# Kernel optimization log

Hardware: AMD Instinct MI355X
Metric: run time of the kernel (lower is better)

## Reference

```python
import jax, jax.numpy as jnp
import numpy as np

ALPHA = 1.0
NEG = -1e20  # boundary value used by the torch module


def _compute_mu(W, alpha):
    """DTW location parameter mu: [B, Na+1, Nb+1].
    mu[i,j] = alpha*W[i-1,j-1] + logsumexp(mu[i-1,j], mu[i,j-1], mu[i-1,j-1]).
    Row-wise scan (outer over i) with an inner scan over j for the
    left-dependency; fully vectorized over batch.
    """
    B, Na, Nb = W.shape
    aW = alpha * W  # [B, Na, Nb]
    # row 0: mu[:,0,0]=0, mu[:,0,1:]=-1e20
    row0 = jnp.concatenate([jnp.zeros((B, 1), W.dtype),
                            jnp.full((B, Nb), NEG, W.dtype)], axis=1)

    def row_step(prev_row, w_row):  # prev_row [B, Nb+1], w_row [B, Nb]
        up = prev_row[:, 1:]    # mu[i-1, j]   for j=1..Nb -> [B, Nb]
        diag = prev_row[:, :-1]  # mu[i-1, j-1]            -> [B, Nb]

        def col_step(left, inp):
            u, d, w = inp  # each [B]
            val = w + jax.nn.logsumexp(jnp.stack([u, left, d], axis=0), axis=0)
            return val, val

        left0 = jnp.full((B,), NEG, W.dtype)  # mu[i, 0] = -1e20
        xs = (up.T, diag.T, w_row.T)          # scan over Nb
        _, vals = jax.lax.scan(col_step, left0, xs)  # [Nb, B]
        new_row = jnp.concatenate([jnp.full((B, 1), NEG, W.dtype), vals.T], axis=1)
        return new_row, new_row

    _, rows = jax.lax.scan(row_step, row0, jnp.swapaxes(aW, 0, 1))  # [Na, B, Nb+1]
    mu = jnp.concatenate([row0[:, None, :], jnp.swapaxes(rows, 0, 1)], axis=1)
    return mu  # [B, Na+1, Nb+1]


def _compute_pi(W, mu, mask, alpha):
    """Reduced transition tensor pi: [B, Na, Nb, 3] (softmax over moves)."""
    up = mu[:, :-1, 1:]    # mu[i-1, j]
    left = mu[:, 1:, :-1]  # mu[i, j-1]
    diag = mu[:, :-1, :-1]  # mu[i-1, j-1]
    raw = jnp.stack([up, left, diag], axis=-1) + alpha * W[..., None]
    return jax.nn.softmax(raw, axis=-1) * mask


def setup_inputs() -> dict:
    key = jax.random.key(0)
    k1, _ = jax.random.split(key)
    B, Na, Nb = 64, 384, 384
    W = jax.random.normal(k1, (B, Na, Nb), dtype=jnp.float32)
    mask = jnp.ones((B, Na, Nb, 1), dtype=jnp.float32)
    return {"W": W, "mask": mask}


def reference(W, mask):
    mu = _compute_mu(W, ALPHA)
    pi = _compute_pi(W, mu, mask, ALPHA)
    return (mu, pi)
```

## Files before the change

kernel.cpp:

```cpp
#include <hip/hip_runtime.h>

#define NA 384
#define NB 384
#define NBATCH 64
#define NEGV -1e20f
#define C 8
#define NCW 6
#define TOT_CH 56
#define WPITCH 68
#define LOG2E 1.44269504088896340736f
#define LN2   0.69314718055994530942f

typedef float f4 __attribute__((ext_vector_type(4)));

struct alignas(16) SharedT {
    float stage[2][NCW][64 * 9];
    float wtile[2][NCW][8 * WPITCH];
    float bound[NCW - 1][NB + 1];
    int   progress[NCW - 1];
    int   computed[NCW];
    int   drained[NCW][2];
    int   wready[NCW];
};

__device__ __forceinline__ void loadW8(const float* __restrict__ Wb, int rbase,
                                       int kk, int l, float (&r)[8])
{
    const int rl = l >> 3, cc = l & 7;
    const int colb = 8 * kk + cc;
#pragma unroll
    for (int i = 0; i < 8; ++i) {
        const int row = 8 * i + rl;
        int col = colb - row;
        col = col < 0 ? 0 : (col > NB - 1 ? NB - 1 : col);
        r[i] = Wb[(size_t)(rbase + row) * NB + col];
    }
}

template<bool FULL>
__device__ __forceinline__ void chunk_body(int k, int w, int l,
                                           float& val, float& diag, SharedT& sh)
{
    const int s0 = 1 + k * C;

    {
        volatile int* wr = &sh.wready[w];
        while (*wr < k + 1) { }
        __builtin_amdgcn_sched_barrier(0);
        asm volatile("" ::: "memory");
    }
    const float* wt = &sh.wtile[k & 1][w][0];
    const int wb = (l >> 3) * WPITCH + (l & 7) * 8;
    const f4 wlo = *(const f4*)(wt + wb);
    const f4 whi = *(const f4*)(wt + wb + 4);

    if (k >= 2) {
        volatile int* dr = &sh.drained[w][k & 1];
        while (*dr < k - 2) __builtin_amdgcn_s_sleep(1);
        __builtin_amdgcn_sched_barrier(0);
        asm volatile("" ::: "memory");
    }
    if (w > 0 && s0 <= NB) {
        const int need = (s0 + C - 1 < NB) ? s0 + C - 1 : NB;
        volatile int* pr = &sh.progress[w - 1];
        while (*pr < need) { }
        __builtin_amdgcn_sched_barrier(0);
        asm volatile("" ::: "memory");
    }
    float bnd[C];
    if (w > 0) {
#pragma unroll
        for (int c = 0; c < C; ++c) {
            const int s = s0 + c;
            bnd[c] = sh.bound[w - 1][s <= NB ? s : NB];
        }
    }
    float wc[C];
    wc[0] = wlo.x * LOG2E; wc[1] = wlo.y * LOG2E;
    wc[2] = wlo.z * LOG2E; wc[3] = wlo.w * LOG2E;
    wc[4] = whi.x * LOG2E; wc[5] = whi.y * LOG2E;
    wc[6] = whi.z * LOG2E; wc[7] = whi.w * LOG2E;

    float* st = &sh.stage[k & 1][w][0];
    __builtin_amdgcn_s_setprio(1);
#pragma unroll
    for (int c = 0; c < C; ++c) {
        const int s = s0 + c;
        float upv = __int_as_float(__builtin_amdgcn_update_dpp(
            0, __float_as_int(val), 0x138 , 0xF, 0xF, false));
        if (l == 0) upv = (w > 0 && s <= NB) ? bnd[c] : NEGV;
        const int j = s - l;
        if (FULL || (j >= 1 && j <= NB)) {
            const float m  = fmaxf(fmaxf(upv, val), diag);
            const float eu = exp2f(upv  - m);
            const float el = exp2f(val  - m);
            const float ed = exp2f(diag - m);
            const float nv = wc[c] + m + __log2f(eu + el + ed);
            st[l * 9 + c] = nv;
            if (w < NCW - 1 && l == 63) sh.bound[w][j] = nv;
            diag = upv;
            val  = nv;
        }
    }
    asm volatile("s_waitcnt lgkmcnt(0)" ::: "memory");
    if (l == 63) {
        if (w < NCW - 1) {
            const int done = s0 + C - 1 - 63;
            if (done >= 1) *(volatile int*)&sh.progress[w] = done;
        }
        *(volatile int*)&sh.computed[w] = k + 1;
    }
    __builtin_amdgcn_s_setprio(0);
}

template<bool FULL>
__device__ __forceinline__ void io_iter(int k, int cw, int l,
        const float* __restrict__ Wb, int rbase, float* __restrict__ mub,
        SharedT& sh)
{
    float wreg[8];
    const bool prep = (k + 2 < TOT_CH);
    if (prep) loadW8(Wb, rbase, k + 2, l, wreg);

    volatile int* cp = &sh.computed[cw];
    while (*cp < k + 1) __builtin_amdgcn_s_sleep(1);
    __builtin_amdgcn_sched_barrier(0);
    asm volatile("" ::: "memory");

    const float* st = &sh.stage[k & 1][cw][0];
    float v[8];
    const int lr = l >> 3, cc = l & 7;
#pragma unroll
    for (int q = 0; q < 8; ++q) v[q] = st[(lr + 8 * q) * 9 + cc];
    asm volatile("s_waitcnt lgkmcnt(0)" ::: "memory");
    if (l == 0) *(volatile int*)&sh.drained[cw][k & 1] = k;

    if (prep) {
        float* wt = &sh.wtile[k & 1][cw][0];
#pragma unroll
        for (int i = 0; i < 8; ++i) wt[i * WPITCH + l] = wreg[i];
        asm volatile("s_waitcnt lgkmcnt(0)" ::: "memory");
        if (l == 0) *(volatile int*)&sh.wready[cw] = k + 3;
    }

    const int colbase = k * C;
#pragma unroll
    for (int q = 0; q < 8; ++q) {
        const int lrow = lr + 8 * q;
        const int col  = colbase + cc - lrow;
        if (FULL || (col >= 0 && col < NB))
            mub[(size_t)(rbase + lrow + 1) * (NB + 1) + col + 1] = v[q] * LN2;
    }
}

__global__ __launch_bounds__(768, 1) void dtw_mu(const float* __restrict__ W,
                                                 float* __restrict__ mu)
{
    __shared__ SharedT sh;
    const int b = blockIdx.x, tid = threadIdx.x;
    const int w = tid >> 6, l = tid & 63;
    const float* Wb = W + (size_t)b * NA * NB;
    float* mub = mu + (size_t)b * (NA + 1) * (NB + 1);

    if (tid < 384) {
        mub[tid + 1] = NEGV;
        mub[(size_t)(tid + 1) * (NB + 1)] = NEGV;
    }
    if (tid == 0) mub[0] = 0.0f;
    if (tid < NCW - 1) sh.progress[tid] = 0;
    if (tid < NCW) { sh.computed[tid] = 0; sh.wready[tid] = 0; }
    if (tid < 2 * NCW) sh.drained[tid >> 1][tid & 1] = -1;
    __syncthreads();

    if (w < NCW) {
        const int rbase = w << 6;
        float val  = NEGV;
        float diag = (rbase + l == 0) ? 0.0f : NEGV;
        for (int k = 0; k < 8; ++k)       chunk_body<false>(k, w, l, val, diag, sh);
        for (int k = 8; k < 48; ++k)      chunk_body<true >(k, w, l, val, diag, sh);
        for (int k = 48; k < TOT_CH; ++k) chunk_body<false>(k, w, l, val, diag, sh);
    } else {
        const int cw = w - NCW, rbase = cw << 6;
        float wreg[8];
        loadW8(Wb, rbase, 0, l, wreg);
        {
            float* wt = &sh.wtile[0][cw][0];
#pragma unroll
            for (int i = 0; i < 8; ++i) wt[i * WPITCH + l] = wreg[i];
        }
        loadW8(Wb, rbase, 1, l, wreg);
        {
            float* wt = &sh.wtile[1][cw][0];
#pragma unroll
            for (int i = 0; i < 8; ++i) wt[i * WPITCH + l] = wreg[i];
        }
        asm volatile("s_waitcnt lgkmcnt(0)" ::: "memory");
        if (l == 0) *(volatile int*)&sh.wready[cw] = 2;

        for (int k = 0; k < 8; ++k)       io_iter<false>(k, cw, l, Wb, rbase, mub, sh);
        for (int k = 8; k < 48; ++k)      io_iter<true >(k, cw, l, Wb, rbase, mub, sh);
        for (int k = 48; k < TOT_CH; ++k) io_iter<false>(k, cw, l, Wb, rbase, mub, sh);
    }
}

__global__ __launch_bounds__(256) void dtw_pi(const float* __restrict__ W,
        const float* __restrict__ mask, const float* __restrict__ mu,
        float* __restrict__ pi)
{
    const long long idx = ((long long)blockIdx.x * 256 + threadIdx.x) * 4;
    const int rr = (int)(idx / NB);
    const int jj = (int)(idx - (long long)rr * NB);
    const int b  = rr / NA;
    const int ii = rr - b * NA;
    const float* m0 = mu + (size_t)b * (NA + 1) * (NB + 1)
                         + (size_t)ii * (NB + 1) + jj;
    const float* m1 = m0 + (NB + 1);
    const float d0 = m0[0], d1 = m0[1], d2 = m0[2], d3 = m0[3], d4 = m0[4];
    const float L0 = m1[0], L1 = m1[1], L2 = m1[2], L3 = m1[3], L4 = m1[4];
    const f4 wv = *(const f4*)(W + idx);
    const f4 mk = *(const f4*)(mask + idx);

    const float t0 = wv.x - L1, t1 = wv.y - L2, t2 = wv.z - L3, t3 = wv.w - L4;
    f4 o0, o1, o2;
    o0.x = exp2f((d1 + t0) * LOG2E) * mk.x;
    o0.y = exp2f((L0 + t0) * LOG2E) * mk.x;
    o0.z = exp2f((d0 + t0) * LOG2E) * mk.x;
    o0.w = exp2f((d2 + t1) * LOG2E) * mk.y;
    o1.x = exp2f((L1 + t1) * LOG2E) * mk.y;
    o1.y = exp2f((d1 + t1) * LOG2E) * mk.y;
    o1.z = exp2f((d3 + t2) * LOG2E) * mk.z;
    o1.w = exp2f((L2 + t2) * LOG2E) * mk.z;
    o2.x = exp2f((d2 + t2) * LOG2E) * mk.z;
    o2.y = exp2f((d4 + t3) * LOG2E) * mk.w;
    o2.z = exp2f((L3 + t3) * LOG2E) * mk.w;
    o2.w = exp2f((d3 + t3) * LOG2E) * mk.w;

    f4* po = (f4*)(pi + idx * 3);
    po[0] = o0; po[1] = o1; po[2] = o2;
}

extern "C" void kernel_launch(void* const* d_in, const int* in_sizes, int n_in,
                              void* d_out, int out_size, void* d_ws, size_t ws_size,
                              hipStream_t stream) {
    const float* W    = (const float*)d_in[0];
    const float* mask = (const float*)d_in[1];
    float* mu = (float*)d_out;
    float* pi = mu + (size_t)NBATCH * (NA + 1) * (NB + 1);

    hipLaunchKernelGGL(dtw_mu, dim3(NBATCH), dim3(768), 0, stream, W, mu);

    const int cells  = NBATCH * NA * NB;
    const int blocks = cells / (256 * 4);
    hipLaunchKernelGGL(dtw_pi, dim3(blocks), dim3(256), 0, stream,
                       W, mask, mu, pi);
}
```

Baseline: 164.3 us.

## Deepen W prefetch pipeline to four buffers and prefetch next chunk weights early

The shared W tile ring grows from two to four slots. The IO wavefronts keep two chunks of W in registers and issue global loads five chunks ahead, so load latency is hidden behind more work. The compute wavefronts now wait on wready and read the next chunk's weights at the end of the current chunk, which takes that LDS read off the critical path at the start of each chunk. The cost is more LDS and registers, plus an extra spin-wait at the tail of each chunk.

```diff
diff --git a/kernel.cpp b/kernel.cpp
--- a/kernel.cpp
+++ b/kernel.cpp
@@ -15,7 +15,7 @@
 
 struct alignas(16) SharedT {
     float stage[2][NCW][64 * 9];
-    float wtile[2][NCW][8 * WPITCH];
+    float wtile[4][NCW][8 * WPITCH];
     float bound[NCW - 1][NB + 1];
     int   progress[NCW - 1];
     int   computed[NCW];
@@ -37,22 +37,28 @@
     }
 }
 
+__device__ __forceinline__ void writeWt(float* __restrict__ wt,
+                                        const float (&r)[8], int l) {
+#pragma unroll
+    for (int i = 0; i < 8; ++i) wt[i * WPITCH + l] = r[i];
+}
+
+__device__ __forceinline__ void readWc(const float* __restrict__ wt, int l,
+                                       float (&wc)[8]) {
+    const int wb = (l >> 3) * WPITCH + (l & 7) * 8;
+    const f4 lo = *(const f4*)(wt + wb);
+    const f4 hi = *(const f4*)(wt + wb + 4);
+    wc[0] = lo.x * LOG2E; wc[1] = lo.y * LOG2E;
+    wc[2] = lo.z * LOG2E; wc[3] = lo.w * LOG2E;
+    wc[4] = hi.x * LOG2E; wc[5] = hi.y * LOG2E;
+    wc[6] = hi.z * LOG2E; wc[7] = hi.w * LOG2E;
+}
+
 template<bool FULL>
 __device__ __forceinline__ void chunk_body(int k, int w, int l,
-                                           float& val, float& diag, SharedT& sh)
+        float (&wc)[8], float& val, float& diag, SharedT& sh)
 {
     const int s0 = 1 + k * C;
-
-    {
-        volatile int* wr = &sh.wready[w];
-        while (*wr < k + 1) { }
-        __builtin_amdgcn_sched_barrier(0);
-        asm volatile("" ::: "memory");
-    }
-    const float* wt = &sh.wtile[k & 1][w][0];
-    const int wb = (l >> 3) * WPITCH + (l & 7) * 8;
-    const f4 wlo = *(const f4*)(wt + wb);
-    const f4 whi = *(const f4*)(wt + wb + 4);
 
     if (k >= 2) {
         volatile int* dr = &sh.drained[w][k & 1];
@@ -75,11 +81,6 @@
             bnd[c] = sh.bound[w - 1][s <= NB ? s : NB];
         }
     }
-    float wc[C];
-    wc[0] = wlo.x * LOG2E; wc[1] = wlo.y * LOG2E;
-    wc[2] = wlo.z * LOG2E; wc[3] = wlo.w * LOG2E;
-    wc[4] = whi.x * LOG2E; wc[5] = whi.y * LOG2E;
-    wc[6] = whi.z * LOG2E; wc[7] = whi.w * LOG2E;
 
     float* st = &sh.stage[k & 1][w][0];
     __builtin_amdgcn_s_setprio(1);
@@ -111,17 +112,21 @@
         *(volatile int*)&sh.computed[w] = k + 1;
     }
     __builtin_amdgcn_s_setprio(0);
+
+    if (k + 1 < TOT_CH) {
+        volatile int* wr = &sh.wready[w];
+        while (*wr < k + 2) { }
+        __builtin_amdgcn_sched_barrier(0);
+        asm volatile("" ::: "memory");
+        readWc(&sh.wtile[(k + 1) & 3][w][0], l, wc);
+    }
 }
 
 template<bool FULL>
 __device__ __forceinline__ void io_iter(int k, int cw, int l,
         const float* __restrict__ Wb, int rbase, float* __restrict__ mub,
-        SharedT& sh)
-{
-    float wreg[8];
-    const bool prep = (k + 2 < TOT_CH);
-    if (prep) loadW8(Wb, rbase, k + 2, l, wreg);
-
+        float (&wreg)[8], SharedT& sh)
+{
     volatile int* cp = &sh.computed[cw];
     while (*cp < k + 1) __builtin_amdgcn_s_sleep(1);
     __builtin_amdgcn_sched_barrier(0);
@@ -135,12 +140,11 @@
     asm volatile("s_waitcnt lgkmcnt(0)" ::: "memory");
     if (l == 0) *(volatile int*)&sh.drained[cw][k & 1] = k;
 
-    if (prep) {
-        float* wt = &sh.wtile[k & 1][cw][0];
-#pragma unroll
-        for (int i = 0; i < 8; ++i) wt[i * WPITCH + l] = wreg[i];
+    if (k + 3 < TOT_CH) {
+        writeWt(&sh.wtile[(k + 3) & 3][cw][0], wreg, l);
         asm volatile("s_waitcnt lgkmcnt(0)" ::: "memory");
-        if (l == 0) *(volatile int*)&sh.wready[cw] = k + 3;
+        if (l == 0) *(volatile int*)&sh.wready[cw] = k + 4;
+        if (k + 5 < TOT_CH) loadW8(Wb, rbase, k + 5, l, wreg);
     }
 
     const int colbase = k * C;
@@ -176,30 +180,43 @@
         const int rbase = w << 6;
         float val  = NEGV;
         float diag = (rbase + l == 0) ? 0.0f : NEGV;
-        for (int k = 0; k < 8; ++k)       chunk_body<false>(k, w, l, val, diag, sh);
-        for (int k = 8; k < 48; ++k)      chunk_body<true >(k, w, l, val, diag, sh);
-        for (int k = 48; k < TOT_CH; ++k) chunk_body<false>(k, w, l, val, diag, sh);
+        float wc[8];
+        {
+            volatile int* wr = &sh.wready[w];
+            while (*wr < 1) { }
+            __builtin_amdgcn_sched_barrier(0);
+            asm volatile("" ::: "memory");
+            readWc(&sh.wtile[0][w][0], l, wc);
+        }
+        for (int k = 0; k < 8; ++k)       chunk_body<false>(k, w, l, wc, val, diag, sh);
+        for (int k = 8; k < 48; ++k)      chunk_body<true >(k, w, l, wc, val, diag, sh);
+        for (int k = 48; k < TOT_CH; ++k) chunk_body<false>(k, w, l, wc, val, diag, sh);
     } else {
         const int cw = w - NCW, rbase = cw << 6;
-        float wreg[8];
-        loadW8(Wb, rbase, 0, l, wreg);
-        {
-            float* wt = &sh.wtile[0][cw][0];
-#pragma unroll
-            for (int i = 0; i < 8; ++i) wt[i * WPITCH + l] = wreg[i];
-        }
-        loadW8(Wb, rbase, 1, l, wreg);
-        {
-            float* wt = &sh.wtile[1][cw][0];
-#pragma unroll
-            for (int i = 0; i < 8; ++i) wt[i * WPITCH + l] = wreg[i];
-        }
+        float r0[8], r1[8], r2[8], rA[8], rB[8];
+        loadW8(Wb, rbase, 0, l, r0);
+        loadW8(Wb, rbase, 1, l, r1);
+        loadW8(Wb, rbase, 2, l, r2);
+        loadW8(Wb, rbase, 3, l, rA);
+        loadW8(Wb, rbase, 4, l, rB);
+        writeWt(&sh.wtile[0][cw][0], r0, l);
+        writeWt(&sh.wtile[1][cw][0], r1, l);
+        writeWt(&sh.wtile[2][cw][0], r2, l);
         asm volatile("s_waitcnt lgkmcnt(0)" ::: "memory");
-        if (l == 0) *(volatile int*)&sh.wready[cw] = 2;
-
-        for (int k = 0; k < 8; ++k)       io_iter<false>(k, cw, l, Wb, rbase, mub, sh);
-        for (int k = 8; k < 48; ++k)      io_iter<true >(k, cw, l, Wb, rbase, mub, sh);
-        for (int k = 48; k < TOT_CH; ++k) io_iter<false>(k, cw, l, Wb, rbase, mub, sh);
+        if (l == 0) *(volatile int*)&sh.wready[cw] = 3;
+
+        for (int k = 0; k < 8; k += 2) {
+            io_iter<false>(k,     cw, l, Wb, rbase, mub, rA, sh);
+            io_iter<false>(k + 1, cw, l, Wb, rbase, mub, rB, sh);
+        }
+        for (int k = 8; k < 48; k += 2) {
+            io_iter<true >(k,     cw, l, Wb, rbase, mub, rA, sh);
+            io_iter<true >(k + 1, cw, l, Wb, rbase, mub, rB, sh);
+        }
+        for (int k = 48; k < TOT_CH; k += 2) {
+            io_iter<false>(k,     cw, l, Wb, rbase, mub, rA, sh);
+            io_iter<false>(k + 1, cw, l, Wb, rbase, mub, rB, sh);
+        }
     }
 }
 
```

Result: no change. 167.0 us (+1.6%).
